# Performance work log

Hardware: AMD Instinct MI355X
Metric: run time of the kernel (lower is better)

## Reference

```python
import jax, jax.numpy as jnp
import numpy as np

B, S, HQ, HKV, DH = 1, 2048, 32, 8, 128
DE = HQ * DH  # DEmbed = 4096
G = HQ // HKV  # GQA group size = 4


def apply_rope(x, cs):
    # x: [B, S, H, DH]; cs: [2, S, 1, DH//2] (broadcast over B via leading dims)
    d = x.shape[-1] // 2
    x1, x2 = x[..., :d], x[..., d:]
    y1 = x1 * cs[0] + x2 * cs[1]
    y2 = -x1 * cs[1] + x2 * cs[0]
    return jnp.concatenate([y1, y2], axis=-1)


def setup_inputs() -> dict:
    key = jax.random.key(0)
    ks = jax.random.split(key, 5)
    x = jax.random.normal(ks[0], (B, S, DE), dtype=jnp.float32)
    # Precomputed rotary tables, shaped [2, S, 1, DH//2] so they broadcast over [B,S,H,DH//2]
    half = DH // 2
    inv_freq = 1.0 / (10000.0 ** (np.arange(half, dtype=np.float64) / half))
    ang = np.arange(S, dtype=np.float64)[:, None] * inv_freq[None, :]
    cos_sin_RoPE = jnp.asarray(
        np.stack([np.cos(ang), np.sin(ang)])[:, :, None, :], dtype=jnp.float32
    )
    sc = DE ** -0.5
    wq = jax.random.normal(ks[1], (DE, HQ * DH), dtype=jnp.float32) * sc
    wk = jax.random.normal(ks[2], (DE, HKV * DH), dtype=jnp.float32) * sc
    wv = jax.random.normal(ks[3], (DE, HKV * DH), dtype=jnp.float32) * sc
    wo = jax.random.normal(ks[4], (DE, DE), dtype=jnp.float32) * sc
    return {"x": x, "cos_sin_RoPE": cos_sin_RoPE, "wq": wq, "wk": wk, "wv": wv, "wo": wo}


def reference(x, cos_sin_RoPE, wq, wk, wv, wo):
    b, s, _ = x.shape
    q = (x @ wq).reshape(b, s, HQ, DH)
    k = (x @ wk).reshape(b, s, HKV, DH)
    v = (x @ wv).reshape(b, s, HKV, DH)
    q = apply_rope(q, cos_sin_RoPE)
    k = apply_rope(k, cos_sin_RoPE)
    # GQA causal SDPA: group query heads per kv head
    q = q.transpose(0, 2, 1, 3).reshape(b, HKV, G, s, DH)  # [b,kv,g,s,d]
    k = k.transpose(0, 2, 1, 3)  # [b,kv,s,d]
    v = v.transpose(0, 2, 1, 3)  # [b,kv,s,d]
    scale = DH ** -0.5
    scores = jnp.einsum('bkgsd,bktd->bkgst', q, k) * scale  # [b,kv,g,s,s]
    mask = jnp.tril(jnp.ones((s, s), dtype=bool))
    scores = jnp.where(mask, scores, jnp.finfo(scores.dtype).min)
    p = jax.nn.softmax(scores, axis=-1)
    o = jnp.einsum('bkgst,bktd->bkgsd', p, v)  # [b,kv,g,s,d]
    o = o.transpose(0, 3, 1, 2, 4).reshape(b, s, HQ * DH)
    return o @ wo
```

## Files before the change

### kernel.cpp

```cpp
#include <hip/hip_runtime.h>
#include <hip/hip_bf16.h>
#include <cstdint>
#include <cstddef>

typedef __bf16 bf16x8 __attribute__((ext_vector_type(8)));
typedef float floatx4 __attribute__((ext_vector_type(4)));

#define MFMA(a, b, c) __builtin_amdgcn_mfma_f32_16x16x32_bf16((a), (b), (c), 0, 0, 0)
#define WAITVM(N) asm volatile("s_waitcnt vmcnt(" #N ")" ::: "memory")
#define WAITLGKM0() asm volatile("s_waitcnt lgkmcnt(0)" ::: "memory")
#define BARRIER() do { asm volatile("" ::: "memory"); __builtin_amdgcn_s_barrier(); asm volatile("" ::: "memory"); } while (0)
#define SCHEDBAR() __builtin_amdgcn_sched_barrier(0)

__device__ __forceinline__ unsigned short f2bf(float f) {
  unsigned u = __builtin_bit_cast(unsigned, f);
  u += 0x7fffu + ((u >> 16) & 1u);
  return (unsigned short)(u >> 16);
}
__device__ __forceinline__ float bf2f(unsigned short h) {
  unsigned u = ((unsigned)h) << 16;
  return __builtin_bit_cast(float, u);
}
__device__ __forceinline__ float fast_exp2(float x) {
#if __has_builtin(__builtin_amdgcn_exp2f)
  return __builtin_amdgcn_exp2f(x);
#else
  return exp2f(x);
#endif
}

__device__ __forceinline__ void gl2lds16(const unsigned short* g, unsigned short* l) {
  __builtin_amdgcn_global_load_lds(
      (const __attribute__((address_space(1))) unsigned int*)g,
      (__attribute__((address_space(3))) unsigned int*)l, 16, 0, 0);
}

__global__ void convert_f32_bf16(const float* __restrict__ src,
                                 unsigned short* __restrict__ dst, int n4) {
  int i = blockIdx.x * 256 + threadIdx.x;
  if (i >= n4) return;
  float4 f = ((const float4*)src)[i];
  ushort4 o;
  o.x = f2bf(f.x); o.y = f2bf(f.y); o.z = f2bf(f.z); o.w = f2bf(f.w);
  ((ushort4*)dst)[i] = o;
}

__global__ void transpose_f32_bf16(const float* __restrict__ src,
                                   unsigned short* __restrict__ dst, int K, int N) {
  __shared__ float tile[64 * 65];
  int tn = blockIdx.x * 64, tk = blockIdx.y * 64;
  int r = threadIdx.x >> 4;
  int c4 = (threadIdx.x & 15) * 4;
#pragma unroll
  for (int i = 0; i < 4; i++) {
    float4 f = *(const float4*)&src[(size_t)(tk + r + 16 * i) * N + tn + c4];
    float* tr = &tile[(r + 16 * i) * 65 + c4];
    tr[0] = f.x; tr[1] = f.y; tr[2] = f.z; tr[3] = f.w;
  }
  __syncthreads();
#pragma unroll
  for (int i = 0; i < 4; i++) {
    ushort4 o;
    o.x = f2bf(tile[(c4 + 0) * 65 + r + 16 * i]);
    o.y = f2bf(tile[(c4 + 1) * 65 + r + 16 * i]);
    o.z = f2bf(tile[(c4 + 2) * 65 + r + 16 * i]);
    o.w = f2bf(tile[(c4 + 3) * 65 + r + 16 * i]);
    *(ushort4*)&dst[(size_t)(tn + r + 16 * i) * K + tk + c4] = o;
  }
}

template <int MI, int MLO>
__device__ __forceinline__ void mfma_cluster(floatx4 (&acc)[MI][4],
                                             const bf16x8* a, const bf16x8* b) {
  __builtin_amdgcn_s_setprio(1);
#pragma unroll
  for (int mi = 0; mi < 4; ++mi)
#pragma unroll
    for (int ni = 0; ni < 4; ++ni)
      acc[MLO + mi][ni] = MFMA(a[MLO + mi], b[ni], acc[MLO + mi][ni]);
  __builtin_amdgcn_s_setprio(0);
}

template <int MI, bool F32OUT>
__global__ __launch_bounds__(512, 2) void gemm_pipe(
    const unsigned short* __restrict__ A,
    const unsigned short* __restrict__ Bt,
    void* __restrict__ C, int M, int N, int K) {
  constexpr int BM = MI * 32;
  constexpr int NSA = BM / 64;
  __shared__ alignas(16) unsigned short Al[2][BM * 64];
  __shared__ alignas(16) unsigned short Bl[2][256 * 64];
  const int tid = threadIdx.x;
  const int w = tid >> 6, L = tid & 63;
  const int lr = L & 15, lg = L >> 4;
  const int bm = blockIdx.y * BM, bn = blockIdx.x * 256;
  const int wm = (w >> 2) * (MI * 16);
  const int wn = (w & 3) * 64;
  const int NT = K >> 6;

  const int srow = tid >> 3, spcg = tid & 7;
  const unsigned short* Ag = &A[(size_t)(bm + srow) * K + ((spcg ^ (srow & 7)) * 8)];
  const unsigned short* Bg = &Bt[(size_t)(bn + srow) * K + ((spcg ^ (srow & 7)) * 8)];
  unsigned short* AlT = &Al[0][0] + tid * 8;
  unsigned short* BlT = &Bl[0][0] + tid * 8;

#pragma unroll
  for (int t = 0; t < 2; ++t) {
#pragma unroll
    for (int j = 0; j < NSA; ++j)
      gl2lds16(Ag + (size_t)(j * 64) * K + t * 64, AlT + t * (BM * 64) + j * 4096);
#pragma unroll
    for (int j = 0; j < 4; ++j)
      gl2lds16(Bg + (size_t)(j * 64) * K + t * 64, BlT + t * (256 * 64) + j * 4096);
  }

  floatx4 acc[MI][4] = {};

  if constexpr (MI == 8) WAITVM(8); else WAITVM(6);
  BARRIER();

  for (int T = 0; T < NT; ++T) {
    const int b = T & 1;
    const unsigned short* Ab = &Al[b][0];
    const unsigned short* Bb = &Bl[b][0];
    bf16x8 a0[MI], a1[MI], b0[4], b1[4];
#pragma unroll
    for (int mi = 0; mi < MI; ++mi)
      a0[mi] = *(const bf16x8*)&Ab[(wm + mi * 16 + lr) * 64 + ((lg ^ (lr & 7)) * 8)];
#pragma unroll
    for (int ni = 0; ni < 4; ++ni)
      b0[ni] = *(const bf16x8*)&Bb[(wn + ni * 16 + lr) * 64 + ((lg ^ (lr & 7)) * 8)];
#pragma unroll
    for (int mi = 0; mi < MI; ++mi)
      a1[mi] = *(const bf16x8*)&Ab[(wm + mi * 16 + lr) * 64 + (((4 + lg) ^ (lr & 7)) * 8)];
#pragma unroll
    for (int ni = 0; ni < 4; ++ni)
      b1[ni] = *(const bf16x8*)&Bb[(wn + ni * 16 + lr) * 64 + (((4 + lg) ^ (lr & 7)) * 8)];

    const bool st = (T + 2) < NT;
    const size_t kofs = (size_t)(T + 2) * 64;
    unsigned short* Ad = AlT + b * (BM * 64);
    unsigned short* Bd = BlT + b * (256 * 64);

    if constexpr (MI == 8) {
      mfma_cluster<8, 0>(acc, a0, b0);
      WAITLGKM0();
      BARRIER(); SCHEDBAR();
      if (st) {
        gl2lds16(Ag + kofs, Ad);
        gl2lds16(Ag + (size_t)64 * K + kofs, Ad + 4096);
        gl2lds16(Ag + (size_t)128 * K + kofs, Ad + 8192);
      }
      mfma_cluster<8, 4>(acc, a0, b0);
      BARRIER(); SCHEDBAR();
      if (st) {
        gl2lds16(Ag + (size_t)192 * K + kofs, Ad + 12288);
        gl2lds16(Bg + kofs, Bd);
        gl2lds16(Bg + (size_t)64 * K + kofs, Bd + 4096);
      }
      mfma_cluster<8, 0>(acc, a1, b1);
      BARRIER(); SCHEDBAR();
      if (st) {
        gl2lds16(Bg + (size_t)128 * K + kofs, Bd + 8192);
        gl2lds16(Bg + (size_t)192 * K + kofs, Bd + 12288);
      }
      mfma_cluster<8, 4>(acc, a1, b1);
      if (st) { WAITVM(8); } else if (T + 1 < NT) { WAITVM(0); }
      BARRIER(); SCHEDBAR();
    } else {
      mfma_cluster<4, 0>(acc, a0, b0);
      WAITLGKM0();
      BARRIER(); SCHEDBAR();
      if (st) {
        gl2lds16(Ag + kofs, Ad);
        gl2lds16(Ag + (size_t)64 * K + kofs, Ad + 4096);
        gl2lds16(Bg + kofs, Bd);
        gl2lds16(Bg + (size_t)64 * K + kofs, Bd + 4096);
        gl2lds16(Bg + (size_t)128 * K + kofs, Bd + 8192);
        gl2lds16(Bg + (size_t)192 * K + kofs, Bd + 12288);
      }
      mfma_cluster<4, 0>(acc, a1, b1);
      if (st) { WAITVM(6); } else if (T + 1 < NT) { WAITVM(0); }
      BARRIER(); SCHEDBAR();
    }
  }

#pragma unroll
  for (int mi = 0; mi < MI; ++mi) {
#pragma unroll
    for (int ni = 0; ni < 4; ++ni) {
#pragma unroll
      for (int r = 0; r < 4; ++r) {
        size_t row = bm + wm + mi * 16 + lg * 4 + r;
        size_t col = bn + wn + ni * 16 + lr;
        float v = acc[mi][ni][r];
        if constexpr (F32OUT) ((float*)C)[row * N + col] = v;
        else ((unsigned short*)C)[row * N + col] = f2bf(v);
      }
    }
  }
}

__global__ void rope_kernel(unsigned short* __restrict__ X, const float* __restrict__ cs,
                            int H, int rowStride, int colOff, float scale) {
  int idx = blockIdx.x * 256 + threadIdx.x;
  int dg = idx & 15;
  int h = (idx >> 4) % H;
  int s = idx / (16 * H);
  size_t base = (size_t)s * rowStride + colOff + (size_t)h * 128 + dg * 4;
  ushort4 xa = *(const ushort4*)&X[base];
  ushort4 xb = *(const ushort4*)&X[base + 64];
  float4 c = *(const float4*)&cs[s * 64 + dg * 4];
  float4 sn = *(const float4*)&cs[2048 * 64 + s * 64 + dg * 4];
  ushort4 oa, ob;
  {
    float x1 = bf2f(xa.x), x2 = bf2f(xb.x);
    oa.x = f2bf((x1 * c.x + x2 * sn.x) * scale);
    ob.x = f2bf((x2 * c.x - x1 * sn.x) * scale);
  }
  {
    float x1 = bf2f(xa.y), x2 = bf2f(xb.y);
    oa.y = f2bf((x1 * c.y + x2 * sn.y) * scale);
    ob.y = f2bf((x2 * c.y - x1 * sn.y) * scale);
  }
  {
    float x1 = bf2f(xa.z), x2 = bf2f(xb.z);
    oa.z = f2bf((x1 * c.z + x2 * sn.z) * scale);
    ob.z = f2bf((x2 * c.z - x1 * sn.z) * scale);
  }
  {
    float x1 = bf2f(xa.w), x2 = bf2f(xb.w);
    oa.w = f2bf((x1 * c.w + x2 * sn.w) * scale);
    ob.w = f2bf((x2 * c.w - x1 * sn.w) * scale);
  }
  *(ushort4*)&X[base] = oa;
  *(ushort4*)&X[base + 64] = ob;
}

__global__ void v_transpose(const unsigned short* __restrict__ QKV,
                            unsigned short* __restrict__ Vt) {
  __shared__ unsigned short tile[32][33];
  int h = blockIdx.z;
  int s0 = blockIdx.x * 32, d0 = blockIdx.y * 32;
  int c = threadIdx.x & 31, r0 = threadIdx.x >> 5;
#pragma unroll
  for (int i = 0; i < 32; i += 8)
    tile[r0 + i][c] = QKV[(size_t)(s0 + r0 + i) * 6144 + 5120 + h * 128 + d0 + c];
  __syncthreads();
#pragma unroll
  for (int i = 0; i < 32; i += 8)
    Vt[(size_t)(h * 128 + d0 + r0 + i) * 2048 + s0 + c] = tile[c][r0 + i];
}

__global__ __launch_bounds__(256) void flash_kernel(
    const unsigned short* __restrict__ QKV,
    const unsigned short* __restrict__ Vt,
    unsigned short* __restrict__ O) {
  constexpr int PSTR = 72;
  __shared__ alignas(16) unsigned short Klds[64 * 128];
  __shared__ alignas(16) unsigned short Vlds[128 * 64];
  __shared__ alignas(16) unsigned short Plds[4 * 32 * PSTR];
  const int tid = threadIdx.x, w = tid >> 6, L = tid & 63;
  const int lr = L & 15, lg = L >> 4;
  const int bid = blockIdx.x;
  const int hk = bid & 7;
  const int hp = (bid >> 3) & 1;
  const int qb = 31 - (bid >> 4);
  const int hq = hk * 4 + hp * 2 + (w & 1);
  const int qr0 = qb * 64 + (w >> 1) * 32;
  const unsigned short* Kg = QKV + 4096;

  const int k_row = tid >> 4, k_lcg = tid & 15;
  const unsigned short* KgT = &Kg[(size_t)k_row * 6144 + hk * 128 + ((k_lcg ^ (k_row & 15)) * 8)];
  unsigned short* KlT = &Klds[k_row * 128 + k_lcg * 8];
  const int v_row = tid >> 3, v_lcg = tid & 7;
  const unsigned short* VgT = &Vt[(size_t)(hk * 128 + v_row) * 2048 + ((v_lcg ^ (v_row & 7)) * 8)];
  unsigned short* VlT = &Vlds[v_row * 64 + v_lcg * 8];

  bf16x8 qf[2][4];
#pragma unroll
  for (int mi = 0; mi < 2; mi++)
#pragma unroll
    for (int c = 0; c < 4; c++)
      qf[mi][c] = *(const bf16x8*)&QKV[(size_t)(qr0 + mi * 16 + lr) * 6144 + hq * 128 + c * 32 + lg * 8];

  floatx4 oacc[2][8] = {};
  float l_lane[2][4] = {};
  unsigned short* pw = &Plds[w * 32 * PSTR];

  for (int t = 0; t <= qb; t++) {
    const int kv0 = t * 64;
    __syncthreads();
#pragma unroll
    for (int i = 0; i < 4; i++) {
      gl2lds16(KgT + (size_t)(kv0 + i * 16) * 6144, KlT + i * 16 * 128);
      gl2lds16(VgT + kv0 + (size_t)(i * 32) * 2048, VlT + i * 32 * 64);
    }
    __syncthreads();

#pragma unroll
    for (int nt = 0; nt < 4; nt++) {
      bf16x8 kf[4];
#pragma unroll
      for (int c = 0; c < 4; c++)
        kf[c] = *(const bf16x8*)&Klds[(nt * 16 + lr) * 128 + (((c * 4 + lg) ^ lr) * 8)];
      floatx4 sc[2];
#pragma unroll
      for (int mi = 0; mi < 2; mi++) {
        floatx4 a = {};
#pragma unroll
        for (int c = 0; c < 4; c++) a = MFMA(qf[mi][c], kf[c], a);
        sc[mi] = a;
      }
      if (t == qb) {
#pragma unroll
        for (int mi = 0; mi < 2; mi++)
#pragma unroll
          for (int r = 0; r < 4; r++)
            if (kv0 + nt * 16 + lr > qr0 + mi * 16 + lg * 4 + r) sc[mi][r] = -3e38f;
      }
#pragma unroll
      for (int mi = 0; mi < 2; mi++)
#pragma unroll
        for (int r = 0; r < 4; r++) {
          float p = fast_exp2(sc[mi][r]);
          l_lane[mi][r] += p;
          pw[(mi * 16 + lg * 4 + r) * PSTR + nt * 16 + lr] = f2bf(p);
        }
    }

    bf16x8 pf[2][2];
#pragma unroll
    for (int mi = 0; mi < 2; mi++)
#pragma unroll
      for (int c = 0; c < 2; c++)
        pf[mi][c] = *(const bf16x8*)&pw[(mi * 16 + lr) * PSTR + c * 32 + lg * 8];

#pragma unroll
    for (int n = 0; n < 8; n++) {
#pragma unroll
      for (int c = 0; c < 2; c++) {
        bf16x8 vf = *(const bf16x8*)&Vlds[(n * 16 + lr) * 64 + (((c * 4 + lg) ^ (lr & 7)) * 8)];
#pragma unroll
        for (int mi = 0; mi < 2; mi++) oacc[mi][n] = MFMA(pf[mi][c], vf, oacc[mi][n]);
      }
    }
  }

  float linv[2][4];
#pragma unroll
  for (int mi = 0; mi < 2; mi++)
#pragma unroll
    for (int r = 0; r < 4; r++) {
      float l = l_lane[mi][r];
      l += __shfl_xor(l, 1);
      l += __shfl_xor(l, 2);
      l += __shfl_xor(l, 4);
      l += __shfl_xor(l, 8);
      linv[mi][r] = 1.0f / l;
    }

#pragma unroll
  for (int mi = 0; mi < 2; mi++)
#pragma unroll
    for (int n = 0; n < 8; n++)
#pragma unroll
      for (int r = 0; r < 4; r++) {
        size_t row = qr0 + mi * 16 + lg * 4 + r;
        size_t col = (size_t)hq * 128 + n * 16 + lr;
        O[row * 4096 + col] = f2bf(oacc[mi][n][r] * linv[mi][r]);
      }
}

extern "C" void kernel_launch(void* const* d_in, const int* in_sizes, int n_in,
                              void* d_out, int out_size, void* d_ws, size_t ws_size,
                              hipStream_t stream) {
  const float* x  = (const float*)d_in[0];
  const float* cs = (const float*)d_in[1];
  const float* wq = (const float*)d_in[2];
  const float* wk = (const float*)d_in[3];
  const float* wv = (const float*)d_in[4];
  const float* wo = (const float*)d_in[5];
  float* out = (float*)d_out;

  char* ws = (char*)d_ws;
  unsigned short* xb   = (unsigned short*)(ws);
  unsigned short* wqt  = (unsigned short*)(ws + 16777216);
  unsigned short* wkt  = (unsigned short*)(ws + 50331648);
  unsigned short* wvt  = (unsigned short*)(ws + 58720256);
  unsigned short* wot  = (unsigned short*)(ws + 67108864);
  unsigned short* QKVb = (unsigned short*)(ws + 100663296);
  unsigned short* Vtb  = (unsigned short*)(ws + 125829120);
  unsigned short* Ob   = xb;

  convert_f32_bf16<<<8192, 256, 0, stream>>>(x, xb, 2097152);
  transpose_f32_bf16<<<dim3(64, 64), 256, 0, stream>>>(wq, wqt, 4096, 4096);
  transpose_f32_bf16<<<dim3(16, 64), 256, 0, stream>>>(wk, wkt, 4096, 1024);
  transpose_f32_bf16<<<dim3(16, 64), 256, 0, stream>>>(wv, wvt, 4096, 1024);
  transpose_f32_bf16<<<dim3(64, 64), 256, 0, stream>>>(wo, wot, 4096, 4096);

  gemm_pipe<8, false><<<dim3(24, 8), 512, 0, stream>>>(xb, wqt, QKVb, 2048, 6144, 4096);

  rope_kernel<<<4096, 256, 0, stream>>>(QKVb, cs, 32, 6144, 0, 0.12751743f);
  rope_kernel<<<1024, 256, 0, stream>>>(QKVb, cs, 8, 6144, 4096, 1.0f);

  v_transpose<<<dim3(64, 4, 8), 256, 0, stream>>>(QKVb, Vtb);

  flash_kernel<<<512, 256, 0, stream>>>(QKVb, Vtb, Ob);

  gemm_pipe<4, true><<<dim3(16, 16), 512, 0, stream>>>(Ob, wot, out, 2048, 4096, 4096);
}
```

Baseline: 495.2 us.

## Retile GEMMs to 256-row tiles with swizzled 1D grid and split A loads

Restructures the pipelined bf16 GEMM so each block covers 256 rows by NI*64 columns (192 for QKV, 128 for the output projection), launched as a 1D grid of 256 blocks with an XCD-aware block-index swizzle. The k-loop is reorganized into four MFMA phases that interleave LDS fragment reads and global-to-LDS prefetches differently. The aim is to balance the 256 CUs with exactly 256 tiles, improve L2 locality across chiplets, and overlap loads with MFMAs. Each wave now holds 8xNI accumulators, and the added barriers could lengthen the critical path.

```diff
diff --git a/kernel.cpp b/kernel.cpp
--- a/kernel.cpp
+++ b/kernel.cpp
@@ -69,129 +69,136 @@
   }
 }
 
-template <int MI, int MLO>
-__device__ __forceinline__ void mfma_cluster(floatx4 (&acc)[MI][4],
-                                             const bf16x8* a, const bf16x8* b) {
-  __builtin_amdgcn_s_setprio(1);
-#pragma unroll
-  for (int mi = 0; mi < 4; ++mi)
-#pragma unroll
-    for (int ni = 0; ni < 4; ++ni)
-      acc[MLO + mi][ni] = MFMA(a[MLO + mi], b[ni], acc[MLO + mi][ni]);
-  __builtin_amdgcn_s_setprio(0);
-}
-
-template <int MI, bool F32OUT>
+template <int NI, bool F32OUT>
 __global__ __launch_bounds__(512, 2) void gemm_pipe(
     const unsigned short* __restrict__ A,
     const unsigned short* __restrict__ Bt,
     void* __restrict__ C, int M, int N, int K) {
-  constexpr int BM = MI * 32;
-  constexpr int NSA = BM / 64;
-  __shared__ alignas(16) unsigned short Al[2][BM * 64];
-  __shared__ alignas(16) unsigned short Bl[2][256 * 64];
+  constexpr int BN = NI * 64;
+  __shared__ alignas(16) unsigned short Al[2][256 * 64];
+  __shared__ alignas(16) unsigned short Bl[2][BN * 64];
   const int tid = threadIdx.x;
   const int w = tid >> 6, L = tid & 63;
-  const int lr = L & 15, lg = L >> 4;
-  const int bm = blockIdx.y * BM, bn = blockIdx.x * 256;
-  const int wm = (w >> 2) * (MI * 16);
-  const int wn = (w & 3) * 64;
+  const int lr = L & 15, lg = L >> 4, lr7 = lr & 7;
+  const int nbx = N / BN;
+  const int sw = (blockIdx.x & 7) * ((int)gridDim.x >> 3) + (blockIdx.x >> 3);
+  const int bn = (sw % nbx) * BN;
+  const int bm = (sw / nbx) * 256;
+  const int wm128 = (w >> 2) * 128;
+  const int wn = (w & 3) * (NI * 16);
   const int NT = K >> 6;
 
-  const int srow = tid >> 3, spcg = tid & 7;
-  const unsigned short* Ag = &A[(size_t)(bm + srow) * K + ((spcg ^ (srow & 7)) * 8)];
-  const unsigned short* Bg = &Bt[(size_t)(bn + srow) * K + ((spcg ^ (srow & 7)) * 8)];
+  const int srow = tid >> 3, scg = tid & 7;
+  const unsigned short* Ag = &A[(size_t)(bm + srow) * K + ((scg ^ (srow & 7)) * 8)];
+  const unsigned short* Bg = &Bt[(size_t)(bn + srow) * K + ((scg ^ (srow & 7)) * 8)];
   unsigned short* AlT = &Al[0][0] + tid * 8;
   unsigned short* BlT = &Bl[0][0] + tid * 8;
 
 #pragma unroll
   for (int t = 0; t < 2; ++t) {
 #pragma unroll
-    for (int j = 0; j < NSA; ++j)
-      gl2lds16(Ag + (size_t)(j * 64) * K + t * 64, AlT + t * (BM * 64) + j * 4096);
-#pragma unroll
-    for (int j = 0; j < 4; ++j)
-      gl2lds16(Bg + (size_t)(j * 64) * K + t * 64, BlT + t * (256 * 64) + j * 4096);
-  }
-
-  floatx4 acc[MI][4] = {};
-
-  if constexpr (MI == 8) WAITVM(8); else WAITVM(6);
+    for (int c = 0; c < 4; ++c)
+      gl2lds16(Ag + (size_t)(c * 64) * K + t * 64, AlT + t * (256 * 64) + c * 4096);
+#pragma unroll
+    for (int c = 0; c < NI; ++c)
+      gl2lds16(Bg + (size_t)(c * 64) * K + t * 64, BlT + t * (BN * 64) + c * 4096);
+  }
+
+  floatx4 acc[8][NI] = {};
+
+  if constexpr (NI == 3) WAITVM(7); else WAITVM(6);
   BARRIER();
 
   for (int T = 0; T < NT; ++T) {
     const int b = T & 1;
     const unsigned short* Ab = &Al[b][0];
     const unsigned short* Bb = &Bl[b][0];
-    bf16x8 a0[MI], a1[MI], b0[4], b1[4];
-#pragma unroll
-    for (int mi = 0; mi < MI; ++mi)
-      a0[mi] = *(const bf16x8*)&Ab[(wm + mi * 16 + lr) * 64 + ((lg ^ (lr & 7)) * 8)];
-#pragma unroll
-    for (int ni = 0; ni < 4; ++ni)
-      b0[ni] = *(const bf16x8*)&Bb[(wn + ni * 16 + lr) * 64 + ((lg ^ (lr & 7)) * 8)];
-#pragma unroll
-    for (int mi = 0; mi < MI; ++mi)
-      a1[mi] = *(const bf16x8*)&Ab[(wm + mi * 16 + lr) * 64 + (((4 + lg) ^ (lr & 7)) * 8)];
-#pragma unroll
-    for (int ni = 0; ni < 4; ++ni)
-      b1[ni] = *(const bf16x8*)&Bb[(wn + ni * 16 + lr) * 64 + (((4 + lg) ^ (lr & 7)) * 8)];
-
     const bool st = (T + 2) < NT;
     const size_t kofs = (size_t)(T + 2) * 64;
-    unsigned short* Ad = AlT + b * (BM * 64);
-    unsigned short* Bd = BlT + b * (256 * 64);
-
-    if constexpr (MI == 8) {
-      mfma_cluster<8, 0>(acc, a0, b0);
-      WAITLGKM0();
-      BARRIER(); SCHEDBAR();
-      if (st) {
-        gl2lds16(Ag + kofs, Ad);
-        gl2lds16(Ag + (size_t)64 * K + kofs, Ad + 4096);
-        gl2lds16(Ag + (size_t)128 * K + kofs, Ad + 8192);
-      }
-      mfma_cluster<8, 4>(acc, a0, b0);
-      BARRIER(); SCHEDBAR();
-      if (st) {
-        gl2lds16(Ag + (size_t)192 * K + kofs, Ad + 12288);
-        gl2lds16(Bg + kofs, Bd);
-        gl2lds16(Bg + (size_t)64 * K + kofs, Bd + 4096);
-      }
-      mfma_cluster<8, 0>(acc, a1, b1);
-      BARRIER(); SCHEDBAR();
-      if (st) {
-        gl2lds16(Bg + (size_t)128 * K + kofs, Bd + 8192);
-        gl2lds16(Bg + (size_t)192 * K + kofs, Bd + 12288);
-      }
-      mfma_cluster<8, 4>(acc, a1, b1);
-      if (st) { WAITVM(8); } else if (T + 1 < NT) { WAITVM(0); }
-      BARRIER(); SCHEDBAR();
-    } else {
-      mfma_cluster<4, 0>(acc, a0, b0);
-      WAITLGKM0();
-      BARRIER(); SCHEDBAR();
-      if (st) {
-        gl2lds16(Ag + kofs, Ad);
-        gl2lds16(Ag + (size_t)64 * K + kofs, Ad + 4096);
-        gl2lds16(Bg + kofs, Bd);
-        gl2lds16(Bg + (size_t)64 * K + kofs, Bd + 4096);
-        gl2lds16(Bg + (size_t)128 * K + kofs, Bd + 8192);
-        gl2lds16(Bg + (size_t)192 * K + kofs, Bd + 12288);
-      }
-      mfma_cluster<4, 0>(acc, a1, b1);
-      if (st) { WAITVM(6); } else if (T + 1 < NT) { WAITVM(0); }
-      BARRIER(); SCHEDBAR();
-    }
-  }
-
-#pragma unroll
-  for (int mi = 0; mi < MI; ++mi) {
-#pragma unroll
-    for (int ni = 0; ni < 4; ++ni) {
+    unsigned short* Ad = AlT + b * (256 * 64);
+    unsigned short* Bd = BlT + b * (BN * 64);
+    bf16x8 a0[4][2], a1[4][2], bq[2][NI];
+
+#pragma unroll
+    for (int mi = 0; mi < 4; ++mi) {
+      a0[mi][0] = *(const bf16x8*)&Ab[(wm128 + mi * 16 + lr) * 64 + ((lg ^ lr7) * 8)];
+      a0[mi][1] = *(const bf16x8*)&Ab[(wm128 + mi * 16 + lr) * 64 + (((4 + lg) ^ lr7) * 8)];
+    }
+#pragma unroll
+    for (int ni = 0; ni < NI; ++ni)
+      bq[0][ni] = *(const bf16x8*)&Bb[(wn + ni * 16 + lr) * 64 + ((lg ^ lr7) * 8)];
+    BARRIER(); WAITLGKM0(); SCHEDBAR();
+    __builtin_amdgcn_s_setprio(1);
+#pragma unroll
+    for (int mi = 0; mi < 4; ++mi)
+#pragma unroll
+      for (int ni = 0; ni < NI; ++ni)
+        acc[mi][ni] = MFMA(a0[mi][0], bq[0][ni], acc[mi][ni]);
+    __builtin_amdgcn_s_setprio(0);
+    BARRIER();
+
+#pragma unroll
+    for (int ni = 0; ni < NI; ++ni)
+      bq[1][ni] = *(const bf16x8*)&Bb[(wn + ni * 16 + lr) * 64 + (((4 + lg) ^ lr7) * 8)];
+#pragma unroll
+    for (int mi = 0; mi < 4; ++mi)
+      a1[mi][0] = *(const bf16x8*)&Ab[(wm128 + 64 + mi * 16 + lr) * 64 + ((lg ^ lr7) * 8)];
+    if (st) {
+      gl2lds16(Ag + kofs, Ad);
+      gl2lds16(Ag + (size_t)128 * K + kofs, Ad + 2 * 4096);
+    }
+    BARRIER(); WAITLGKM0(); SCHEDBAR();
+    __builtin_amdgcn_s_setprio(1);
+#pragma unroll
+    for (int mi = 0; mi < 4; ++mi)
+#pragma unroll
+      for (int ni = 0; ni < NI; ++ni)
+        acc[mi][ni] = MFMA(a0[mi][1], bq[1][ni], acc[mi][ni]);
+    __builtin_amdgcn_s_setprio(0);
+    BARRIER();
+
+#pragma unroll
+    for (int mi = 0; mi < 4; ++mi)
+      a1[mi][1] = *(const bf16x8*)&Ab[(wm128 + 64 + mi * 16 + lr) * 64 + (((4 + lg) ^ lr7) * 8)];
+    if (st) {
+#pragma unroll
+      for (int c = 0; c < NI; ++c)
+        gl2lds16(Bg + (size_t)(c * 64) * K + kofs, Bd + c * 4096);
+    }
+    BARRIER(); WAITLGKM0(); SCHEDBAR();
+    __builtin_amdgcn_s_setprio(1);
+#pragma unroll
+    for (int mi = 0; mi < 4; ++mi)
+#pragma unroll
+      for (int ni = 0; ni < NI; ++ni)
+        acc[4 + mi][ni] = MFMA(a1[mi][0], bq[0][ni], acc[4 + mi][ni]);
+    __builtin_amdgcn_s_setprio(0);
+    BARRIER();
+
+    if (st) {
+      gl2lds16(Ag + (size_t)64 * K + kofs, Ad + 4096);
+      gl2lds16(Ag + (size_t)192 * K + kofs, Ad + 3 * 4096);
+    }
+    BARRIER(); WAITLGKM0(); SCHEDBAR();
+    __builtin_amdgcn_s_setprio(1);
+#pragma unroll
+    for (int mi = 0; mi < 4; ++mi)
+#pragma unroll
+      for (int ni = 0; ni < NI; ++ni)
+        acc[4 + mi][ni] = MFMA(a1[mi][1], bq[1][ni], acc[4 + mi][ni]);
+    __builtin_amdgcn_s_setprio(0);
+    if constexpr (NI == 3) { if (st) { WAITVM(7); } else { WAITVM(0); } }
+    else                   { if (st) { WAITVM(6); } else { WAITVM(0); } }
+    BARRIER();
+  }
+
+#pragma unroll
+  for (int mi = 0; mi < 8; ++mi) {
+#pragma unroll
+    for (int ni = 0; ni < NI; ++ni) {
 #pragma unroll
       for (int r = 0; r < 4; ++r) {
-        size_t row = bm + wm + mi * 16 + lg * 4 + r;
+        size_t row = bm + wm128 + mi * 16 + lg * 4 + r;
         size_t col = bn + wn + ni * 16 + lr;
         float v = acc[mi][ni][r];
         if constexpr (F32OUT) ((float*)C)[row * N + col] = v;
@@ -399,7 +406,7 @@
   transpose_f32_bf16<<<dim3(16, 64), 256, 0, stream>>>(wv, wvt, 4096, 1024);
   transpose_f32_bf16<<<dim3(64, 64), 256, 0, stream>>>(wo, wot, 4096, 4096);
 
-  gemm_pipe<8, false><<<dim3(24, 8), 512, 0, stream>>>(xb, wqt, QKVb, 2048, 6144, 4096);
+  gemm_pipe<3, false><<<256, 512, 0, stream>>>(xb, wqt, QKVb, 2048, 6144, 4096);
 
   rope_kernel<<<4096, 256, 0, stream>>>(QKVb, cs, 32, 6144, 0, 0.12751743f);
   rope_kernel<<<1024, 256, 0, stream>>>(QKVb, cs, 8, 6144, 4096, 1.0f);
@@ -408,5 +415,5 @@
 
   flash_kernel<<<512, 256, 0, stream>>>(QKVb, Vtb, Ob);
 
-  gemm_pipe<4, true><<<dim3(16, 16), 512, 0, stream>>>(Ob, wot, out, 2048, 4096, 4096);
-}
+  gemm_pipe<2, true><<<256, 512, 0, stream>>>(Ob, wot, out, 2048, 4096, 4096);
+}
```

New measurement: 555.4 us. 12.2% more time.
